# Performance work log

Hardware: AMD Instinct MI355X
Metric: run time of the kernel (lower is better)

The kernel has to match this reference:

```python
import jax, jax.numpy as jnp
import numpy as np

K = 11          # k_size in the original module
HALF = K // 2   # 5
N_SIGNAL = 33554432  # 2**25 elements, 128 MB fp32


def setup_inputs() -> dict:
    key = jax.random.key(0)
    k1, _ = jax.random.split(key)
    x = jax.random.normal(k1, (N_SIGNAL,), dtype=jnp.float32)
    # learned parameter of Dilation1D(s=1.5)
    scale = jnp.asarray(1.5, dtype=jnp.float32)
    return {"x": x, "scale": scale}


def reference(x, scale):
    # parabolic structuring element: z = -5..5, h = -z^2 / (4*scale)
    z = jnp.linspace(-(K // 2), K // 2, K, dtype=jnp.float32)  # torch: -k//2+1 .. k//2 == -5..5
    h = -(z * z) / (4.0 * scale)  # [K]

    n = x.shape[0]
    pad = jnp.full((HALF,), -jnp.inf, dtype=x.dtype)
    xp = jnp.concatenate([pad, x, pad])  # [n + K - 1], -inf edge handling == original branches

    # out[r] = max_j ( x[r - HALF + j] + h[j] )  (max-plus / grayscale dilation)
    out = xp[0:n] + h[0]
    for j in range(1, K):  # fixed small K, unrolled window — no data-dim loop
        out = jnp.maximum(out, xp[j:j + n] + h[j])
    return out
```

## Files before the change

### kernel.cpp

```cpp
#include <hip/hip_runtime.h>
#include <math.h>
#include <stdint.h>


typedef float f32x4 __attribute__((ext_vector_type(4)));

#define BLOCK   256
#define QPT     4
#define TILE_Q  (BLOCK * QPT)
#define HALO_Q  2
#define STAGE_Q (TILE_Q + 2 * HALO_Q)

__device__ __forceinline__ void gload_lds16(const f32x4* g, f32x4* l) {
    __builtin_amdgcn_global_load_lds(
        (const __attribute__((address_space(1))) uint32_t*)(uintptr_t)g,
        (__attribute__((address_space(3))) uint32_t*)(uintptr_t)l,
        16, 0, 0);
}

__global__ __launch_bounds__(BLOCK) void dilate1d_kernel(
    const f32x4* __restrict__ x4,
    const float* __restrict__ scale_p,
    f32x4*       __restrict__ out4,
    int n4)
{
    __shared__ f32x4 smem[STAGE_Q];

    const float NEG  = -INFINITY;
    const f32x4 NEG4 = {NEG, NEG, NEG, NEG};

    const int Q0   = blockIdx.x * TILE_Q;
    const int g0   = Q0 - HALO_Q;
    const int wid  = threadIdx.x >> 6;

    const bool interior = (g0 >= 0) && (g0 + STAGE_Q <= n4);
    if (interior) {
#pragma unroll
        for (int t = 0; t < QPT; ++t) {
            int idx = t * BLOCK + threadIdx.x;
            gload_lds16(x4 + g0 + idx,
                        smem + t * BLOCK + wid * 64);
        }
        if (threadIdx.x < 2 * HALO_Q) {
            gload_lds16(x4 + g0 + TILE_Q + threadIdx.x,
                        smem + TILE_Q);
        }
    } else {
#pragma unroll
        for (int t = 0; t <= QPT; ++t) {
            int idx = threadIdx.x + t * BLOCK;
            if (idx < STAGE_Q) {
                int g = g0 + idx;
                smem[idx] = (g >= 0 && g < n4) ? x4[g] : NEG4;
            }
        }
    }
    __syncthreads();

    const float r4s = 1.0f / (4.0f * scale_p[0]);
    const float hp1 = -1.0f  * r4s;
    const float hp2 = -4.0f  * r4s;
    const float hp3 = -9.0f  * r4s;
    const float hp4 = -16.0f * r4s;
    const float hp5 = -25.0f * r4s;

#pragma unroll
    for (int t = 0; t < QPT; ++t) {
        int idx = threadIdx.x + t * BLOCK;
        int q   = Q0 + idx;
        if (q >= n4) break;

        float w[20];
#pragma unroll
        for (int r = 0; r < 5; ++r) {
            f32x4 v = smem[idx + r];
            w[4 * r + 0] = v.x;
            w[4 * r + 1] = v.y;
            w[4 * r + 2] = v.z;
            w[4 * r + 3] = v.w;
        }

        f32x4 o;
#pragma unroll
        for (int i = 0; i < 4; ++i) {
            int c = 8 + i;
            float m = w[c];
            m = fmaxf(m, hp1 + fmaxf(w[c - 1], w[c + 1]));
            m = fmaxf(m, hp2 + fmaxf(w[c - 2], w[c + 2]));
            m = fmaxf(m, hp3 + fmaxf(w[c - 3], w[c + 3]));
            m = fmaxf(m, hp4 + fmaxf(w[c - 4], w[c + 4]));
            m = fmaxf(m, hp5 + fmaxf(w[c - 5], w[c + 5]));
            o[i] = m;
        }
        __builtin_nontemporal_store(o, out4 + q);
    }
}

extern "C" void kernel_launch(void* const* d_in, const int* in_sizes, int n_in,
                              void* d_out, int out_size, void* d_ws, size_t ws_size,
                              hipStream_t stream) {
    const float* x       = (const float*)d_in[0];
    const float* scale_p = (const float*)d_in[1];
    float*       out     = (float*)d_out;

    int n  = in_sizes[0];
    int n4 = n / 4;

    int grid = (n4 + TILE_Q - 1) / TILE_Q;

    dilate1d_kernel<<<grid, BLOCK, 0, stream>>>(
        (const f32x4*)x, scale_p, (f32x4*)out, n4);
}
```

Measured before the change: 230.0 us.

## Double-buffer LDS staging and process eight tiles per block

Each block now walks eight consecutive tiles and prefetches the next tile into a second LDS buffer while it computes the current one, using a barrier between tiles. The goal is to hide global-to-LDS load latency behind the max-plus compute and to amortize the per-block setup, such as reading scale and deriving the constants. In exchange the grid shrinks eightfold, to about 1024 blocks, and LDS use doubles. That can reduce the number of waves in flight for what is a bandwidth-bound streaming kernel.

```diff
diff --git a/kernel.cpp b/kernel.cpp
--- a/kernel.cpp
+++ b/kernel.cpp
@@ -10,6 +10,7 @@
 #define TILE_Q  (BLOCK * QPT)
 #define HALO_Q  2
 #define STAGE_Q (TILE_Q + 2 * HALO_Q)
+#define TPB     8
 
 __device__ __forceinline__ void gload_lds16(const f32x4* g, f32x4* l) {
     __builtin_amdgcn_global_load_lds(
@@ -22,40 +23,39 @@
     const f32x4* __restrict__ x4,
     const float* __restrict__ scale_p,
     f32x4*       __restrict__ out4,
-    int n4)
+    int n4,
+    int ntiles)
 {
-    __shared__ f32x4 smem[STAGE_Q];
+    __shared__ f32x4 smem[2][STAGE_Q];
 
     const float NEG  = -INFINITY;
     const f32x4 NEG4 = {NEG, NEG, NEG, NEG};
+    const int   wid  = threadIdx.x >> 6;
 
-    const int Q0   = blockIdx.x * TILE_Q;
-    const int g0   = Q0 - HALO_Q;
-    const int wid  = threadIdx.x >> 6;
-
-    const bool interior = (g0 >= 0) && (g0 + STAGE_Q <= n4);
-    if (interior) {
+    auto stage = [&](int b, int tile) {
+        const int g0 = tile * TILE_Q - HALO_Q;
+        const bool interior = (g0 >= 0) && (g0 + STAGE_Q <= n4);
+        if (interior) {
 #pragma unroll
-        for (int t = 0; t < QPT; ++t) {
-            int idx = t * BLOCK + threadIdx.x;
-            gload_lds16(x4 + g0 + idx,
-                        smem + t * BLOCK + wid * 64);
-        }
-        if (threadIdx.x < 2 * HALO_Q) {
-            gload_lds16(x4 + g0 + TILE_Q + threadIdx.x,
-                        smem + TILE_Q);
-        }
-    } else {
+            for (int t = 0; t < QPT; ++t) {
+                gload_lds16(x4 + g0 + t * BLOCK + threadIdx.x,
+                            &smem[b][t * BLOCK + wid * 64]);
+            }
+            if (threadIdx.x < 2 * HALO_Q) {
+                gload_lds16(x4 + g0 + TILE_Q + threadIdx.x,
+                            &smem[b][TILE_Q]);
+            }
+        } else {
 #pragma unroll
-        for (int t = 0; t <= QPT; ++t) {
-            int idx = threadIdx.x + t * BLOCK;
-            if (idx < STAGE_Q) {
-                int g = g0 + idx;
-                smem[idx] = (g >= 0 && g < n4) ? x4[g] : NEG4;
+            for (int t = 0; t <= QPT; ++t) {
+                int idx = threadIdx.x + t * BLOCK;
+                if (idx < STAGE_Q) {
+                    int g = g0 + idx;
+                    smem[b][idx] = (g >= 0 && g < n4) ? x4[g] : NEG4;
+                }
             }
         }
-    }
-    __syncthreads();
+    };
 
     const float r4s = 1.0f / (4.0f * scale_p[0]);
     const float hp1 = -1.0f  * r4s;
@@ -64,35 +64,53 @@
     const float hp4 = -16.0f * r4s;
     const float hp5 = -25.0f * r4s;
 
+    const int t0   = blockIdx.x * TPB;
+    const int tend = (t0 + TPB < ntiles) ? t0 + TPB : ntiles;
+    if (t0 >= ntiles) return;
+
+    stage(0, t0);
+    __syncthreads();
+
+    int p = 0;
+    for (int tile = t0; tile < tend; ++tile) {
+        if (tile + 1 < tend) stage(p ^ 1, tile + 1);
+
+        const int Q0 = tile * TILE_Q;
 #pragma unroll
-    for (int t = 0; t < QPT; ++t) {
-        int idx = threadIdx.x + t * BLOCK;
-        int q   = Q0 + idx;
-        if (q >= n4) break;
+        for (int t = 0; t < QPT; ++t) {
+            int idx = threadIdx.x + t * BLOCK;
+            int q   = Q0 + idx;
+            if (q >= n4) break;
 
-        float w[20];
+            float w[20];
 #pragma unroll
-        for (int r = 0; r < 5; ++r) {
-            f32x4 v = smem[idx + r];
-            w[4 * r + 0] = v.x;
-            w[4 * r + 1] = v.y;
-            w[4 * r + 2] = v.z;
-            w[4 * r + 3] = v.w;
+            for (int r = 0; r < 5; ++r) {
+                f32x4 v = smem[p][idx + r];
+                w[4 * r + 0] = v.x;
+                w[4 * r + 1] = v.y;
+                w[4 * r + 2] = v.z;
+                w[4 * r + 3] = v.w;
+            }
+
+            f32x4 o;
+#pragma unroll
+            for (int i = 0; i < 4; ++i) {
+                int c = 8 + i;
+                float m = w[c];
+                m = fmaxf(m, hp1 + fmaxf(w[c - 1], w[c + 1]));
+                m = fmaxf(m, hp2 + fmaxf(w[c - 2], w[c + 2]));
+                m = fmaxf(m, hp3 + fmaxf(w[c - 3], w[c + 3]));
+                m = fmaxf(m, hp4 + fmaxf(w[c - 4], w[c + 4]));
+                m = fmaxf(m, hp5 + fmaxf(w[c - 5], w[c + 5]));
+                o[i] = m;
+            }
+            __builtin_nontemporal_store(o, out4 + q);
         }
 
-        f32x4 o;
-#pragma unroll
-        for (int i = 0; i < 4; ++i) {
-            int c = 8 + i;
-            float m = w[c];
-            m = fmaxf(m, hp1 + fmaxf(w[c - 1], w[c + 1]));
-            m = fmaxf(m, hp2 + fmaxf(w[c - 2], w[c + 2]));
-            m = fmaxf(m, hp3 + fmaxf(w[c - 3], w[c + 3]));
-            m = fmaxf(m, hp4 + fmaxf(w[c - 4], w[c + 4]));
-            m = fmaxf(m, hp5 + fmaxf(w[c - 5], w[c + 5]));
-            o[i] = m;
+        if (tile + 1 < tend) {
+            __syncthreads();
+            p ^= 1;
         }
-        __builtin_nontemporal_store(o, out4 + q);
     }
 }
 
@@ -103,11 +121,11 @@
     const float* scale_p = (const float*)d_in[1];
     float*       out     = (float*)d_out;
 
-    int n  = in_sizes[0];
-    int n4 = n / 4;
+    int n      = in_sizes[0];
+    int n4     = n / 4;
+    int ntiles = (n4 + TILE_Q - 1) / TILE_Q;
+    int blocks = (ntiles + TPB - 1) / TPB;
 
-    int grid = (n4 + TILE_Q - 1) / TILE_Q;
-
-    dilate1d_kernel<<<grid, BLOCK, 0, stream>>>(
-        (const f32x4*)x, scale_p, (f32x4*)out, n4);
+    dilate1d_kernel<<<blocks, BLOCK, 0, stream>>>(
+        (const f32x4*)x, scale_p, (f32x4*)out, n4, ntiles);
 }
```

After: 241.5 us. +5.0%, slower.
